# Optimization experiments

Measured on AMD Instinct MI355X. Metric: run time of the kernel, lower is better.

Reference implementation:

```python
import jax, jax.numpy as jnp
import numpy as np
from jax import lax

B, T, H, W, C = 32, 250, 28, 28, 1
CLASSES, IPC = 25, 10
UNITS = 512
MEM_CELLS = CLASSES * IPC  # 250
CELL = 64
HEADS = 4
FEAT = 2 * 2 * 32          # conv output flattened = 128
XDIM = FEAT + CLASSES      # 153
IN_LSTM = XDIM + HEADS * CELL  # 409
EPS_BN = 1e-3


def setup_inputs() -> dict:
    key = jax.random.key(0)
    ks = iter(jax.random.split(key, 40))
    s = 0.02
    d = {}
    d['images'] = jax.random.normal(next(ks), (B, T, H, W, C), jnp.float32)
    d['previous_labels'] = jax.random.randint(next(ks), (B, T), 0, CLASSES, jnp.int32)
    # conv stack
    for i, (ci, co) in enumerate([(1, 8), (8, 16), (16, 32)], start=1):
        d[f'k{i}'] = jax.random.normal(next(ks), (3, 3, ci, co), jnp.float32) * s
        d[f'cb{i}'] = jnp.zeros((co,), jnp.float32)
        d[f'g{i}'] = jnp.ones((co,), jnp.float32)
        d[f'be{i}'] = jnp.zeros((co,), jnp.float32)
        d[f'mm{i}'] = jnp.zeros((co,), jnp.float32)
        d[f'mv{i}'] = jnp.ones((co,), jnp.float32)
    # LSTM cell (keras gate order i,f,g,o)
    d['Wx'] = jax.random.normal(next(ks), (IN_LSTM, 4 * UNITS), jnp.float32) * s
    d['Wh'] = jax.random.normal(next(ks), (UNITS, 4 * UNITS), jnp.float32) * s
    d['bl'] = jnp.zeros((4 * UNITS,), jnp.float32)
    # parameters dense -> (read_heads+1)*cell_size, tanh
    d['Wp'] = jax.random.normal(next(ks), (UNITS, (HEADS + 1) * CELL), jnp.float32) * s
    d['bp'] = jnp.zeros(((HEADS + 1) * CELL,), jnp.float32)
    # output layer: Dense(units, tanh) on concat(h, read_value)
    d['Wo'] = jax.random.normal(next(ks), (UNITS + HEADS * CELL, UNITS), jnp.float32) * s
    d['bo'] = jnp.zeros((UNITS,), jnp.float32)
    # final classifier
    d['Wf'] = jax.random.normal(next(ks), (UNITS, CLASSES), jnp.float32) * s
    d['bf'] = jnp.zeros((CLASSES,), jnp.float32)
    return d


def _conv_bn_relu(x, k, cb, g, be, mm, mv):
    y = lax.conv_general_dilated(x, k, (2, 2), 'VALID',
                                 dimension_numbers=('NHWC', 'HWIO', 'NHWC')) + cb
    y = (y - mm) * g * lax.rsqrt(mv + EPS_BN) + be  # inference BN
    return jax.nn.relu(y)


def _l2n(x):
    return x * lax.rsqrt(jnp.maximum(jnp.sum(x * x, axis=-1, keepdims=True), 1e-12))


def _forward(images, previous_labels, k1, cb1, g1, be1, mm1, mv1,
             k2, cb2, g2, be2, mm2, mv2, k3, cb3, g3, be3, mm3, mv3,
             Wx, Wh, bl, Wp, bp, Wo, bo, Wf, bf):
    x = images.reshape(B * T, H, W, C)
    x = _conv_bn_relu(x, k1, cb1, g1, be1, mm1, mv1)
    x = _conv_bn_relu(x, k2, cb2, g2, be2, mm2, mv2)
    x = _conv_bn_relu(x, k3, cb3, g3, be3, mm3, mv3)
    x = x.reshape(B, T, FEAT)
    oh = jax.nn.one_hot(previous_labels, CLASSES, dtype=x.dtype)
    x = jnp.concatenate([x, oh], axis=-1)  # [B, T, XDIM]

    def step(carry, xt):
        h, c, rv, mem = carry
        inp = jnp.concatenate([xt, rv], axis=-1)
        z = inp @ Wx + h @ Wh + bl
        zi, zf, zg, zo = jnp.split(z, 4, axis=-1)
        i, f, g = jax.nn.sigmoid(zi), jax.nn.sigmoid(zf), jnp.tanh(zg)
        o = jax.nn.sigmoid(zo)
        c = f * c + i * g
        h = o * jnp.tanh(c)
        hid = jnp.tanh(h @ Wp + bp)
        wv = hid[:, :CELL]                                # write value
        keys = hid[:, CELL:].reshape(B, HEADS, CELL)
        att = jnp.einsum('brs,bms->brm', _l2n(keys), _l2n(mem))
        w = jax.nn.softmax(att, axis=-1)
        rv = jnp.einsum('brm,bms->brs', w, mem).reshape(B, HEADS * CELL)
        mem = jnp.concatenate([wv[:, None, :], mem[:, :-1]], axis=1)  # shift write
        out = jnp.tanh(jnp.concatenate([h, rv], axis=-1) @ Wo + bo)
        return (h, c, rv, mem), out

    carry0 = (jnp.zeros((B, UNITS)), jnp.zeros((B, UNITS)),
              jnp.zeros((B, HEADS * CELL)), jnp.zeros((B, MEM_CELLS, CELL)))
    _, ys = lax.scan(step, carry0, jnp.swapaxes(x, 0, 1))  # ys: [T, B, UNITS]
    rnn_out = jnp.swapaxes(ys, 0, 1)
    return jax.nn.softmax(rnn_out @ Wf + bf, axis=-1)


def reference(images, previous_labels, k1, cb1, g1, be1, mm1, mv1,
              k2, cb2, g2, be2, mm2, mv2, k3, cb3, g3, be3, mm3, mv3,
              Wx, Wh, bl, Wp, bp, Wo, bo, Wf, bf):
    return _forward(images, previous_labels, k1, cb1, g1, be1, mm1, mv1,
                    k2, cb2, g2, be2, mm2, mv2, k3, cb3, g3, be3, mm3, mv3,
                    Wx, Wh, bl, Wp, bp, Wo, bo, Wf, bf)
```

## Files before the change

### kernel.cpp

```cpp
#include <hip/hip_runtime.h>


constexpr size_t OFF_FEATP  = 0;
constexpr size_t OFF_WXI    = OFF_FEATP + (size_t)8000 * 128;
constexpr size_t OFF_WHI    = OFF_WXI + (size_t)409 * 2048;
constexpr size_t OFF_BLI    = OFF_WHI + (size_t)512 * 2048;
constexpr size_t OFF_ZP2    = OFF_BLI + 2048;
constexpr size_t OFF_OH2A   = OFF_ZP2 + 262144;
constexpr size_t OFF_OH2B   = OFF_OH2A + 65536;
constexpr size_t OFF_OUTPRE2= OFF_OH2B + 65536;
constexpr size_t OFF_HT2    = OFF_OUTPRE2 + 32768;
constexpr size_t OFF_HTT2   = OFF_HT2 + 65536;
constexpr size_t OFF_RVT2   = OFF_HTT2 + 65536;
constexpr size_t OFF_WVP2   = OFF_RVT2 + 32768;
constexpr size_t OFF_BAR    = OFF_WVP2 + 16384;
constexpr size_t OFF_WPT    = OFF_BAR + 4096;
constexpr size_t WS_FLOATS  = OFF_WPT + (size_t)163840;

constexpr int DYN_FLOATS = 34816;
constexpr int DYN_BYTES  = DYN_FLOATS * 4;

constexpr int COH = 0, COP = 512, CCO = 1024, CRING = 1536;

__device__ __forceinline__ float sigm(float x) { return 1.f / (1.f + __expf(-x)); }

typedef int iv2 __attribute__((ext_vector_type(2)));
typedef int iv4 __attribute__((ext_vector_type(4)));

__device__ __forceinline__ void st_pair(float* base, size_t pidx, float v, int tag) {
  unsigned long long u = (unsigned long long)__float_as_uint(v) |
                         ((unsigned long long)(unsigned)tag << 32);
  __hip_atomic_store((unsigned long long*)(base + 2 * pidx), u,
                     __ATOMIC_RELAXED, __HIP_MEMORY_SCOPE_AGENT);
}
__device__ __forceinline__ float spin_pair(const float* base, size_t pidx, int tag) {
  const iv2* p = (const iv2*)(base + 2 * pidx);
  iv2 v;
  for (;;) {
    asm volatile("global_load_dwordx2 %0, %1, off sc0 sc1\n\ts_waitcnt vmcnt(0)"
                 : "=&v"(v) : "v"(p) : "memory");
    if (v[1] == tag) break;
    __builtin_amdgcn_s_sleep(1);
  }
  return __int_as_float(v[0]);
}
__device__ __forceinline__ float2 spin_pair2(const float* base, size_t pidx, int tag) {
  const iv4* p = (const iv4*)(base + 2 * pidx);
  iv4 v;
  for (;;) {
    asm volatile("global_load_dwordx4 %0, %1, off sc0 sc1\n\ts_waitcnt vmcnt(0)"
                 : "=&v"(v) : "v"(p) : "memory");
    if (v[1] == tag && v[3] == tag) break;
    __builtin_amdgcn_s_sleep(1);
  }
  return {__int_as_float(v[0]), __int_as_float(v[2])};
}
__device__ __forceinline__ float2 spin_pair_2addr(const float* a, const float* b, int tag) {
  const iv2* pa = (const iv2*)a;
  const iv2* pb = (const iv2*)b;
  iv2 x, y;
  for (;;) {
    asm volatile(
        "global_load_dwordx2 %0, %2, off sc0 sc1\n\t"
        "global_load_dwordx2 %1, %3, off sc0 sc1\n\t"
        "s_waitcnt vmcnt(0)"
        : "=&v"(x), "=&v"(y) : "v"(pa), "v"(pb) : "memory");
    if (x[1] == tag && y[1] == tag) break;
    __builtin_amdgcn_s_sleep(1);
  }
  return {__int_as_float(x[0]), __int_as_float(y[0])};
}
__device__ __forceinline__ void ld8i4_sc(const iv4* b0, iv4* v) {
  const iv4 *p0 = b0, *p1 = b0 + 512, *p2 = b0 + 1024, *p3 = b0 + 1536,
            *p4 = b0 + 2048, *p5 = b0 + 2560, *p6 = b0 + 3072, *p7 = b0 + 3584;
  asm volatile(
      "global_load_dwordx4 %0, %8, off sc0 sc1\n\t"
      "global_load_dwordx4 %1, %9, off sc0 sc1\n\t"
      "global_load_dwordx4 %2, %10, off sc0 sc1\n\t"
      "global_load_dwordx4 %3, %11, off sc0 sc1\n\t"
      "global_load_dwordx4 %4, %12, off sc0 sc1\n\t"
      "global_load_dwordx4 %5, %13, off sc0 sc1\n\t"
      "global_load_dwordx4 %6, %14, off sc0 sc1\n\t"
      "global_load_dwordx4 %7, %15, off sc0 sc1\n\t"
      "s_waitcnt vmcnt(0)"
      : "=&v"(v[0]), "=&v"(v[1]), "=&v"(v[2]), "=&v"(v[3]),
        "=&v"(v[4]), "=&v"(v[5]), "=&v"(v[6]), "=&v"(v[7])
      : "v"(p0), "v"(p1), "v"(p2), "v"(p3), "v"(p4), "v"(p5), "v"(p6), "v"(p7)
      : "memory");
}
__device__ __forceinline__ void ld10i4_sc(const iv4* b0, const iv4* z0,
                                          const iv4* z1, iv4* v) {
  const iv4 *p0 = b0, *p1 = b0 + 512, *p2 = b0 + 1024, *p3 = b0 + 1536,
            *p4 = b0 + 2048, *p5 = b0 + 2560, *p6 = b0 + 3072, *p7 = b0 + 3584;
  asm volatile(
      "global_load_dwordx4 %0, %10, off sc0 sc1\n\t"
      "global_load_dwordx4 %1, %11, off sc0 sc1\n\t"
      "global_load_dwordx4 %2, %12, off sc0 sc1\n\t"
      "global_load_dwordx4 %3, %13, off sc0 sc1\n\t"
      "global_load_dwordx4 %4, %14, off sc0 sc1\n\t"
      "global_load_dwordx4 %5, %15, off sc0 sc1\n\t"
      "global_load_dwordx4 %6, %16, off sc0 sc1\n\t"
      "global_load_dwordx4 %7, %17, off sc0 sc1\n\t"
      "global_load_dwordx4 %8, %18, off sc0 sc1\n\t"
      "global_load_dwordx4 %9, %19, off sc0 sc1\n\t"
      "s_waitcnt vmcnt(0)"
      : "=&v"(v[0]), "=&v"(v[1]), "=&v"(v[2]), "=&v"(v[3]), "=&v"(v[4]),
        "=&v"(v[5]), "=&v"(v[6]), "=&v"(v[7]), "=&v"(v[8]), "=&v"(v[9])
      : "v"(p0), "v"(p1), "v"(p2), "v"(p3), "v"(p4), "v"(p5), "v"(p6), "v"(p7),
        "v"(z0), "v"(z1)
      : "memory");
}
__device__ __forceinline__ int sum8_bar(const int* b) {
  int v0, v1, v2, v3, v4, v5, v6, v7;
  asm volatile(
      "global_load_dword %0, %8, off sc0 sc1\n\t"
      "global_load_dword %1, %9, off sc0 sc1\n\t"
      "global_load_dword %2, %10, off sc0 sc1\n\t"
      "global_load_dword %3, %11, off sc0 sc1\n\t"
      "global_load_dword %4, %12, off sc0 sc1\n\t"
      "global_load_dword %5, %13, off sc0 sc1\n\t"
      "global_load_dword %6, %14, off sc0 sc1\n\t"
      "global_load_dword %7, %15, off sc0 sc1\n\t"
      "s_waitcnt vmcnt(0)"
      : "=&v"(v0), "=&v"(v1), "=&v"(v2), "=&v"(v3),
        "=&v"(v4), "=&v"(v5), "=&v"(v6), "=&v"(v7)
      : "v"(b), "v"(b + 64), "v"(b + 128), "v"(b + 192),
        "v"(b + 256), "v"(b + 320), "v"(b + 384), "v"(b + 448)
      : "memory");
  return ((v0 + v1) + (v2 + v3)) + ((v4 + v5) + (v6 + v7));
}

__global__ __launch_bounds__(256) void prep_kernel(const float* __restrict__ Wx,
                                                   const float* __restrict__ Wh,
                                                   const float* __restrict__ bl,
                                                   const float* __restrict__ Wp,
                                                   float* __restrict__ ws) {
  float* WXI = ws + OFF_WXI;
  float* WHI = ws + OFF_WHI;
  float* BLI = ws + OFF_BLI;
  float* WPT = ws + OFF_WPT;
  const int t0 = 409 * 2048;
  const int t1 = t0 + 512 * 2048;
  const int t2 = t1 + 2048;
  const int total = t2 + 163840;
  for (int idx = blockIdx.x * blockDim.x + threadIdx.x; idx < total;
       idx += gridDim.x * blockDim.x) {
    if (idx < t0) {
      int k = idx >> 11, cc = idx & 2047;
      WXI[idx] = Wx[(size_t)k * 2048 + (cc & 3) * 512 + (cc >> 2)];
    } else if (idx < t1) {
      int j = idx - t0;
      int k = j >> 11, cc = j & 2047;
      WHI[j] = Wh[(size_t)k * 2048 + (cc & 3) * 512 + (cc >> 2)];
    } else if (idx < t2) {
      int cc = idx - t1;
      BLI[cc] = bl[(cc & 3) * 512 + (cc >> 2)];
    } else {
      int e = idx - t2;
      int k4 = e / 1280, r = e - k4 * 1280;
      int j = r >> 2, ks = r & 3;
      WPT[e] = Wp[(size_t)(k4 * 4 + ks) * 320 + j];
    }
  }
}

__global__ __launch_bounds__(128) void conv_kernel(
    const float* __restrict__ img,
    const float* __restrict__ k1, const float* __restrict__ cb1, const float* __restrict__ g1,
    const float* __restrict__ be1, const float* __restrict__ mm1, const float* __restrict__ mv1,
    const float* __restrict__ k2, const float* __restrict__ cb2, const float* __restrict__ g2,
    const float* __restrict__ be2, const float* __restrict__ mm2, const float* __restrict__ mv2,
    const float* __restrict__ k3, const float* __restrict__ cb3, const float* __restrict__ g3,
    const float* __restrict__ be3, const float* __restrict__ mm3, const float* __restrict__ mv3,
    float* __restrict__ ws) {
  __shared__ float s_in[784];
  __shared__ float s_y1[13 * 13 * 8];
  __shared__ float s_y2[6 * 6 * 16];
  __shared__ float s_k1[72], s_k2[1152], s_k3[4608];
  __shared__ float s_s1[8], s_b1[8], s_s2[16], s_b2[16], s_s3[32], s_b3[32];
  float* FEATP = ws + OFF_FEATP;
  const int n = blockIdx.x, tid = threadIdx.x;
  const float* ip = img + (size_t)n * 784;
  for (int i = tid; i < 784; i += 128) s_in[i] = ip[i];
  for (int i = tid; i < 72; i += 128) s_k1[i] = k1[i];
  for (int i = tid; i < 1152; i += 128) s_k2[i] = k2[i];
  for (int i = tid; i < 4608; i += 128) s_k3[i] = k3[i];
  if (tid < 8) {
    float s = g1[tid] * rsqrtf(mv1[tid] + 1e-3f);
    s_s1[tid] = s; s_b1[tid] = (cb1[tid] - mm1[tid]) * s + be1[tid];
  } else if (tid >= 32 && tid < 48) {
    int c = tid - 32;
    float s = g2[c] * rsqrtf(mv2[c] + 1e-3f);
    s_s2[c] = s; s_b2[c] = (cb2[c] - mm2[c]) * s + be2[c];
  } else if (tid >= 64 && tid < 96) {
    int c = tid - 64;
    float s = g3[c] * rsqrtf(mv3[c] + 1e-3f);
    s_s3[c] = s; s_b3[c] = (cb3[c] - mm3[c]) * s + be3[c];
  }
  __syncthreads();
  for (int idx = tid; idx < 13 * 13 * 8; idx += 128) {
    int co = idx & 7, pos = idx >> 3;
    int j = pos % 13, i = pos / 13;
    float acc = 0.f;
    #pragma unroll
    for (int ky = 0; ky < 3; ++ky)
      #pragma unroll
      for (int kx = 0; kx < 3; ++kx)
        acc += s_in[(2 * i + ky) * 28 + (2 * j + kx)] * s_k1[(ky * 3 + kx) * 8 + co];
    float v = acc * s_s1[co] + s_b1[co];
    s_y1[idx] = v > 0.f ? v : 0.f;
  }
  __syncthreads();
  for (int idx = tid; idx < 6 * 6 * 16; idx += 128) {
    int co = idx & 15, pos = idx >> 4;
    int j = pos % 6, i = pos / 6;
    float acc = 0.f;
    for (int ky = 0; ky < 3; ++ky)
      for (int kx = 0; kx < 3; ++kx) {
        int base = ((2 * i + ky) * 13 + (2 * j + kx)) * 8;
        int kb = (ky * 3 + kx) * 128 + co;
        #pragma unroll
        for (int ci = 0; ci < 8; ++ci) acc += s_y1[base + ci] * s_k2[kb + ci * 16];
      }
    float v = acc * s_s2[co] + s_b2[co];
    s_y2[idx] = v > 0.f ? v : 0.f;
  }
  __syncthreads();
  for (int idx = tid; idx < 128; idx += 128) {
    int co = idx & 31, pos = idx >> 5;
    int j = pos & 1, i = pos >> 1;
    float acc = 0.f;
    for (int ky = 0; ky < 3; ++ky)
      for (int kx = 0; kx < 3; ++kx) {
        int base = ((2 * i + ky) * 6 + (2 * j + kx)) * 16;
        int kb = (ky * 3 + kx) * 512 + co;
        #pragma unroll
        for (int ci = 0; ci < 16; ++ci) acc += s_y2[base + ci] * s_k3[kb + ci * 32];
      }
    float v = acc * s_s3[co] + s_b3[co];
    FEATP[(size_t)n * 128 + idx] = v > 0.f ? v : 0.f;
  }
}

__global__ __launch_bounds__(512) void lstm_kernel(
    const int* __restrict__ labels,
    const float* __restrict__ Wo, const float* __restrict__ bo,
    const float* __restrict__ Wp, const float* __restrict__ bp,
    const float* __restrict__ Wf, const float* __restrict__ bf,
    float* __restrict__ ws, float* __restrict__ out) {
  extern __shared__ float dyn[];
  const float* FEATP = ws + OFF_FEATP;
  const float* WXI   = ws + OFF_WXI;
  const float* WHI   = ws + OFF_WHI;
  const float* BLI   = ws + OFF_BLI;
  float* ZP2    = ws + OFF_ZP2;
  float* OH2A   = ws + OFF_OH2A;
  float* OH2B   = ws + OFF_OH2B;
  float* OUTPRE2= ws + OFF_OUTPRE2;
  float* HT2    = ws + OFF_HT2;
  float* HTT2   = ws + OFF_HTT2;
  float* RVT2   = ws + OFF_RVT2;
  float* WVP2   = ws + OFF_WVP2;
  const float* WPT = ws + OFF_WPT;
  int*   BARp   = (int*)(ws + OFF_BAR);

  const int bid = blockIdx.x;
  const int tid = threadIdx.x;

  auto waitC = [&](int base, int target) {
    if (tid == 0) {
      while (sum8_bar(BARp + base) < target) {}
    }
    __syncthreads();
  };
  auto bumpC = [&](int base) {
    asm volatile("s_waitcnt vmcnt(0)" ::: "memory");
    __syncthreads();
    if (tid == 0) atomicAdd(&BARp[base + ((bid & 7) << 6)], 1);
  };

  auto stageP = [&](float* dst, const float* srcPairs, int tag) {
    const iv4* sp = (const iv4*)srcPairs + tid;
    iv4 v[8];
    for (;;) {
      ld8i4_sc(sp, v);
      bool ok = true;
      #pragma unroll
      for (int j = 0; j < 8; ++j) ok = ok && (v[j][1] == tag) && (v[j][3] == tag);
      if (ok) break;
      __builtin_amdgcn_s_sleep(2);
    }
    #pragma unroll
    for (int j = 0; j < 8; ++j) {
      int i = (tid + j * 512) << 1;
      float2 f = {__int_as_float(v[j][0]), __int_as_float(v[j][2])};
      *(float2*)&dst[(i >> 5) * 36 + (i & 31)] = f;
    }
  };

  auto E32 = [&](const float* Wm, const float* Am, int K, float* part, float2& r) {
    const int wv = tid >> 6, l = tid & 63;
    const int ksub = l & 1, cg = (l >> 1) & 3, bg = l >> 3;
    const int Kp = K >> 4;
    const int kb = wv * (K >> 3) + ksub * Kp;
    const float* wp = Wm + (size_t)kb * 32 + cg * 8;
    const float* ap = Am + (size_t)kb * 36 + bg * 4;
    float4 acc[8];
    #pragma unroll
    for (int i = 0; i < 8; ++i) acc[i] = {0.f, 0.f, 0.f, 0.f};
    #pragma unroll 4
    for (int kk = 0; kk < Kp; ++kk) {
      float4 w0 = *(const float4*)(wp + kk * 32);
      float4 w1 = *(const float4*)(wp + kk * 32 + 4);
      float4 a  = *(const float4*)(ap + kk * 36);
      float wl[8];
      *(float4*)&wl[0] = w0; *(float4*)&wl[4] = w1;
      #pragma unroll
      for (int i = 0; i < 8; ++i) {
        acc[i].x = fmaf(wl[i], a.x, acc[i].x);
        acc[i].y = fmaf(wl[i], a.y, acc[i].y);
        acc[i].z = fmaf(wl[i], a.z, acc[i].z);
        acc[i].w = fmaf(wl[i], a.w, acc[i].w);
      }
    }
    #pragma unroll
    for (int i = 0; i < 8; ++i) {
      acc[i].x += __shfl_xor(acc[i].x, 1, 64);
      acc[i].y += __shfl_xor(acc[i].y, 1, 64);
      acc[i].z += __shfl_xor(acc[i].z, 1, 64);
      acc[i].w += __shfl_xor(acc[i].w, 1, 64);
    }
    const int ob = (cg * 8) * 36 + bg * 4;
    if (ksub == 0 && wv < 4) {
      float* pb = part + wv * 1152 + ob;
      #pragma unroll
      for (int i = 0; i < 8; ++i) *(float4*)(pb + i * 36) = acc[i];
    }
    __syncthreads();
    if (ksub == 0 && wv >= 4) {
      float* pb = part + (wv - 4) * 1152 + ob;
      #pragma unroll
      for (int i = 0; i < 8; ++i) {
        float4 t = *(float4*)(pb + i * 36);
        t.x += acc[i].x; t.y += acc[i].y; t.z += acc[i].z; t.w += acc[i].w;
        *(float4*)(pb + i * 36) = t;
      }
    }
    __syncthreads();
    const int c = tid & 31, b2 = (tid >> 5) * 2;
    const int o = c * 36 + b2;
    float2 s0 = *(float2*)(part + o);
    float2 s1 = *(float2*)(part + 1152 + o);
    float2 s2 = *(float2*)(part + 2304 + o);
    float2 s3 = *(float2*)(part + 3456 + o);
    r.x = (s0.x + s1.x) + (s2.x + s3.x);
    r.y = (s0.y + s1.y) + (s2.y + s3.y);
  };

  if (bid < 64) {
    const int c0 = bid * 32;
    for (int i = tid; i < 8192; i += 512)
      dyn[i] = WXI[(size_t)(153 + (i >> 5)) * 2048 + c0 + (i & 31)];
    for (int i = tid; i < 4096; i += 512)
      dyn[8192 + i] = WXI[(size_t)(i >> 5) * 2048 + c0 + (i & 31)];
    if (tid < 256) dyn[12288 + tid] = 0.f;
  } else if (bid < 80) {
    const int u0 = (bid - 64) * 32;
    for (int i = tid; i < 8192; i += 512)
      dyn[i] = Wo[(size_t)(512 + (i >> 5)) * 512 + u0 + (i & 31)];
    if (tid < 32) dyn[8192 + tid] = bo[u0 + tid];
  } else if (bid < 144) {
    const int c0 = (bid - 80) * 32;
    for (int i = tid; i < 16384; i += 512)
      dyn[i] = WHI[(size_t)(i >> 5) * 2048 + c0 + (i & 31)];
    if (tid < 32) dyn[16384 + tid] = BLI[c0 + tid];
  } else if (bid < 160) {
    const int u0 = (bid - 144) * 32;
    for (int i = tid; i < 8192; i += 512)
      dyn[i] = Wo[(size_t)(i >> 5) * 512 + u0 + (i & 31)];
  } else if (bid < 176) {
    const int u0 = (bid - 160) * 32;
    for (int i = tid; i < 8192; i += 512)
      dyn[i] = Wo[(size_t)(256 + (i >> 5)) * 512 + u0 + (i & 31)];
  } else if (bid < 240) {
    const int hp = (bid - 176) & 1;
    for (int i = tid; i < 17000; i += 512) dyn[i] = 0.f;
    if (tid < 256) dyn[17000 + tid] = rsqrtf(1e-12f);
    if (tid < 128) dyn[21264 + tid] = bp[64 + hp * 128 + tid];
    if (tid < 64)  dyn[21392 + tid] = bp[tid];
  } else if (bid < 244) {
    const int kh = (bid - 240) >> 1, cp = (bid - 240) & 1;
    for (int i = tid; i < 8192; i += 512) {
      int k = i >> 5, c = i & 31;
      dyn[i] = Wp[(size_t)(kh * 256 + k) * 320 + cp * 32 + c];
    }
  } else if (bid < 252) {
    for (int i = tid; i < 12800; i += 512) dyn[i] = Wf[i];
    if (tid < 25) dyn[12800 + tid] = bf[tid];
  }
  __syncthreads();

  auto azPre = [&](int t) {
    const int c0 = bid * 32;
    const float* zpP = ZP2 + (t & 1) * 131072;
    float* zf = dyn + 27392;
    const int bb = tid >> 4, c2 = tid & 15;
    float2 x = spin_pair2(zpP, (size_t)bb * 2048 + c0 + c2 * 2, t + 1);
    *(float2*)&zf[bb * 32 + c2 * 2] = x;
  };
  auto azGatesMain = [&](int t) {
    const float* rvP = RVT2 + ((t + 1) & 1) * 16384;
    float* Wz = dyn; float* Cst = dyn + 12288; float* rvT = dyn + 12544;
    float* zx = dyn + 26368; float* zf = dyn + 27392; float* part = dyn + 28416;
    stageP(rvT, rvP, t);
    __syncthreads();
    float2 r;
    E32(Wz, rvT, 256, part, r);
    const int c = tid & 31, b2 = (tid >> 5) * 2;
    zf[b2 * 32 + c] += r.x + zx[b2 * 32 + c];
    zf[(b2 + 1) * 32 + c] += r.y + zx[(b2 + 1) * 32 + c];
    __syncthreads();
    if (tid < 256) {
      int u = tid & 7, b = tid >> 3;
      float4 z = *(float4*)(zf + b * 32 + u * 4);
      float ig = sigm(z.x), fg = sigm(z.y), gg = tanhf(z.z), og = sigm(z.w);
      float cc = fg * Cst[b * 8 + u] + ig * gg;
      Cst[b * 8 + u] = cc;
      float hv = og * tanhf(cc);
      st_pair(HT2 + (t & 1) * 32768, (size_t)(bid * 8 + u) * 32 + b, hv, t + 1);
      st_pair(HTT2 + (t & 1) * 32768, (size_t)b * 512 + bid * 8 + u, hv, t + 1);
    }
  };
  auto azX = [&](int tt) {
    float* Wxx = dyn + 8192; float* xT = dyn + 21760;
    float* zx = dyn + 26368; float* part = dyn + 28416;
    for (int i = tid; i < 4096; i += 512) {
      int b = i >> 7, k = i & 127;
      xT[k * 36 + b] = FEATP[((size_t)b * 250 + tt) * 128 + k];
    }
    __syncthreads();
    float2 r;
    E32(Wxx, xT, 128, part, r);
    const int c = tid & 31, b2 = (tid >> 5) * 2;
    zx[b2 * 32 + c] = r.x;
    zx[(b2 + 1) * 32 + c] = r.y;
  };
  auto aoOut = [&](int t) {
    const int u0 = (bid - 64) * 32;
    const float* rvP  = RVT2 + ((t + 1) & 1) * 16384;
    const float* ohaP = OH2A + ((t + 1) & 1) * 32768;
    const float* ohbP = OH2B + ((t + 1) & 1) * 32768;
    float* W = dyn; float* bo_l = dyn + 8192; float* rvT = dyn + 8224;
    float* of = dyn + 17440; float* part = dyn + 18464;
    {
      const int b = tid >> 4, c2 = tid & 15;
      const iv4* rp = (const iv4*)rvP + tid;
      const iv4* za = (const iv4*)ohaP + (b * 256 + (u0 >> 1) + c2);
      const iv4* zb = (const iv4*)ohbP + (b * 256 + (u0 >> 1) + c2);
      iv4 v[10];
      for (;;) {
        ld10i4_sc(rp, za, zb, v);
        bool ok = true;
        #pragma unroll
        for (int j = 0; j < 10; ++j) ok = ok && (v[j][1] == t) && (v[j][3] == t);
        if (ok) break;
        __builtin_amdgcn_s_sleep(2);
      }
      #pragma unroll
      for (int j = 0; j < 8; ++j) {
        int i = (tid + j * 512) << 1;
        float2 f = {__int_as_float(v[j][0]), __int_as_float(v[j][2])};
        *(float2*)&rvT[(i >> 5) * 36 + (i & 31)] = f;
      }
      float2 s = {__int_as_float(v[8][0]) + __int_as_float(v[9][0]),
                  __int_as_float(v[8][2]) + __int_as_float(v[9][2])};
      *(float2*)&of[b * 32 + c2 * 2] = s;
    }
    __syncthreads();
    float2 r;
    E32(W, rvT, 256, part, r);
    const int c = tid & 31, b2 = (tid >> 5) * 2;
    float bv = bo_l[c];
    st_pair(OUTPRE2, (size_t)b2 * 512 + u0 + c, r.x + of[b2 * 32 + c] + bv, t);
    st_pair(OUTPRE2, (size_t)(b2 + 1) * 512 + u0 + c, r.y + of[(b2 + 1) * 32 + c] + bv, t);
  };
  auto zhLab = [&](int s) {
    __syncthreads();
    int* slab = (int*)(dyn + 16416);
    if (tid < 32) slab[tid] = labels[tid * 250 + s];
  };
  auto zhGemm = [&](int s) {
    const int c0 = (bid - 80) * 32;
    const float* htP = HT2 + ((s + 1) & 1) * 32768;
    float* zpD = ZP2 + (s & 1) * 131072;
    float* W = dyn; float* blc = dyn + 16384; int* slab = (int*)(dyn + 16416);
    float* A = dyn + 16448; float* part = dyn + 25664;
    stageP(A, htP, s);
    __syncthreads();
    float2 r1;
    E32(W, A, 256, part, r1);
    __syncthreads();
    stageP(A, htP + 16384, s);
    __syncthreads();
    float2 r2;
    E32(W + 8192, A, 256, part, r2);
    const int c = tid & 31, b2 = (tid >> 5) * 2;
    float base = blc[c];
    int l0 = slab[b2], l1 = slab[b2 + 1];
    st_pair(zpD, (size_t)b2 * 2048 + c0 + c,
            r1.x + r2.x + base + WXI[(size_t)(128 + l0) * 2048 + c0 + c], s + 1);
    st_pair(zpD, (size_t)(b2 + 1) * 2048 + c0 + c,
            r1.y + r2.y + base + WXI[(size_t)(128 + l1) * 2048 + c0 + c], s + 1);
  };
  auto p2Gemm = [&](int t) {
    const float* htP = HT2 + (t & 1) * 32768;
    float* W = dyn; float* A = dyn + 8192; float* part = dyn + 17408;
    const bool isOLr = bid < 160;
    stageP(A, isOLr ? htP : (htP + 16384), t + 1);
    __syncthreads();
    float2 r;
    E32(W, A, 256, part, r);
    const int c = tid & 31, b2 = (tid >> 5) * 2;
    const int u0 = (isOLr ? (bid - 144) : (bid - 160)) * 32;
    float* d = (isOLr ? OH2A : OH2B) + (t & 1) * 32768;
    st_pair(d, (size_t)b2 * 512 + u0 + c, r.x, t + 1);
    st_pair(d, (size_t)(b2 + 1) * 512 + u0 + c, r.y, t + 1);
  };
  auto caOutB = [&](int b, int t) {
    float* WfL = dyn; float* bfL = dyn + 12800;
    float* to = dyn + 12832; float* lp = dyn + 13344; float* lg = dyn + 13744;
    to[tid] = tanhf(spin_pair(OUTPRE2, (size_t)b * 512 + tid, t));
    __syncthreads();
    if (tid < 400) {
      int l = tid % 25, p = tid / 25;
      float s = 0.f;
      #pragma unroll
      for (int q = 0; q < 32; ++q) { int k = p * 32 + q; s += to[k] * WfL[k * 25 + l]; }
      lp[p * 25 + l] = s;
    }
    __syncthreads();
    if (tid < 25) {
      float s = bfL[tid];
      #pragma unroll
      for (int p = 0; p < 16; ++p) s += lp[p * 25 + tid];
      lg[tid] = s;
    }
    __syncthreads();
    if (tid == 0) {
      float mx = lg[0];
      for (int l = 1; l < 25; ++l) mx = fmaxf(mx, lg[l]);
      float ss = 0.f;
      for (int l = 0; l < 25; ++l) ss += __expf(lg[l] - mx);
      lg[25] = mx; lg[26] = 1.f / ss;
    }
    __syncthreads();
    if (tid < 25)
      out[((size_t)b * 250 + (t - 1)) * 25 + tid] = __expf(lg[tid] - lg[25]) * lg[26];
    __syncthreads();
  };

  if (bid < 64) {
    azX(0);
    for (int t = 0; t < 250; ++t) {
      azPre(t);
      if (t >= 2) waitC(COH, 32 * (t - 1));
      azGatesMain(t);
      if (t < 249) azX(t + 1);
    }
  } else if (bid < 80) {
    for (int t = 1; t <= 250; ++t) {
      if (t >= 2) waitC(CCO, 8 * (t - 1));
      aoOut(t);
      bumpC(COP);
    }
  } else if (bid < 144) {
    for (int s = 0; s < 250; ++s) {
      zhLab(s);
      zhGemm(s);
    }
  } else if (bid < 176) {
    for (int t = 0; t < 250; ++t) {
      if (t >= 2) waitC(COP, 16 * (t - 1));
      p2Gemm(t);
      bumpC(COH);
    }
  } else if (bid < 240) {
    float* ring = dyn;
    float* rn   = dyn + 17000;
    float* h_s  = dyn + 17256;
    float* kpart= dyn + 17768;
    float* kv   = dyn + 18280;
    float* kn   = dyn + 18408;
    float* att  = dyn + 18536;
    float* redK = dyn + 19048;
    float* redM = dyn + 19052;
    float* redS = dyn + 19068;
    float* pslab= dyn + 19088;
    float* bpk  = dyn + 21264;
    float* bpw  = dyn + 21392;
    const int b = (bid - 176) >> 1, hp = (bid - 176) & 1;
    const int j = tid & 127, q = tid >> 7;
    const int J = 64 + hp * 128 + j;
    const float4* wbase = (const float4*)WPT + q * 32 * 320 + J;
    for (int t = 0; t < 250; ++t) {
      float4 pf[16];
      #pragma unroll
      for (int i = 0; i < 16; ++i) pf[i] = wbase[i * 320];
      if (t >= 2) waitC(COP, 16 * (t - 1));
      h_s[tid] = spin_pair(HTT2 + (t & 1) * 32768, (size_t)b * 512 + tid, t + 1);
      __syncthreads();
      {
        float a = 0.f;
        #pragma unroll
        for (int i = 0; i < 16; ++i) {
          float4 h4 = *(const float4*)&h_s[q * 128 + i * 4];
          a += pf[i].x * h4.x + pf[i].y * h4.y + pf[i].z * h4.z + pf[i].w * h4.w;
        }
        #pragma unroll 4
        for (int i = 16; i < 32; ++i) {
          float4 w = wbase[i * 320];
          float4 h4 = *(const float4*)&h_s[q * 128 + i * 4];
          a += w.x * h4.x + w.y * h4.y + w.z * h4.z + w.w * h4.w;
        }
        kpart[q * 128 + j] = a;
      }
      __syncthreads();
      if (tid < 128) {
        float kr = kpart[tid] + kpart[128 + tid] + kpart[256 + tid] +
                   kpart[384 + tid] + bpk[tid];
        float v = tanhf(kr);
        kv[tid] = v;
        float pq = v * v;
        #pragma unroll
        for (int off = 32; off; off >>= 1) pq += __shfl_xor(pq, off, 64);
        if ((tid & 63) == 0) redK[tid >> 6] = rsqrtf(fmaxf(pq, 1e-12f));
      }
      __syncthreads();
      if (tid < 128) kn[tid] = kv[tid] * redK[tid >> 6];
      __syncthreads();
      const int start = (250 - t) % 250;
      const int m = tid >> 1, hh = tid & 1;
      {
        float v;
        if (m < 250) {
          int p = start + m; if (p >= 250) p -= 250;
          const float4* c4 = (const float4*)ring + p * 17;
          const float4* k4 = (const float4*)kn + hh * 16;
          float d = 0.f;
          #pragma unroll
          for (int s4 = 0; s4 < 16; ++s4) {
            float4 cc = c4[s4], kk = k4[s4];
            d += cc.x * kk.x + cc.y * kk.y + cc.z * kk.z + cc.w * kk.w;
          }
          v = d * rn[p];
        } else v = -3.0e38f;
        float mx = v;
        #pragma unroll
        for (int off = 2; off <= 32; off <<= 1) mx = fmaxf(mx, __shfl_xor(mx, off, 64));
        if ((tid & 63) < 2) redM[(tid >> 6) * 2 + (tid & 1)] = mx;
        __syncthreads();
        float MX = redM[hh];
        #pragma unroll
        for (int w = 1; w < 8; ++w) MX = fmaxf(MX, redM[w * 2 + hh]);
        float e = (m < 250) ? __expf(v - MX) : 0.f;
        if (m < 250) att[hh * 256 + m] = e;
        float sm = e;
        #pragma unroll
        for (int off = 2; off <= 32; off <<= 1) sm += __shfl_xor(sm, off, 64);
        if ((tid & 63) < 2) redS[(tid >> 6) * 2 + (tid & 1)] = sm;
      }
      __syncthreads();
      {
        int hh2 = tid >> 8, s4 = (tid >> 4) & 15, g = tid & 15;
        float4 a4 = {0.f, 0.f, 0.f, 0.f};
        for (int mm = g; mm < 250; mm += 16) {
          int p = start + mm; if (p >= 250) p -= 250;
          float w = att[hh2 * 256 + mm];
          float4 cc = ((const float4*)ring)[p * 17 + s4];
          a4.x = fmaf(w, cc.x, a4.x); a4.y = fmaf(w, cc.y, a4.y);
          a4.z = fmaf(w, cc.z, a4.z); a4.w = fmaf(w, cc.w, a4.w);
        }
        *(float4*)&pslab[(hh2 * 16 + s4) * 68 + g * 4] = a4;
      }
      __syncthreads();
      if (tid < 128) {
        int hh3 = tid >> 6, s = tid & 63;
        float denom = redS[hh3];
        #pragma unroll
        for (int w = 1; w < 8; ++w) denom += redS[w * 2 + hh3];
        float sum = 0.f;
        #pragma unroll
        for (int g = 0; g < 16; ++g)
          sum += pslab[(hh3 * 16 + (s >> 2)) * 68 + g * 4 + (s & 3)];
        st_pair(RVT2 + (t & 1) * 16384,
                (size_t)((2 * hp + hh3) * 64 + s) * 32 + b, sum / denom, t + 1);
      }
      __syncthreads();
      {
        int ip = start + 249; if (ip >= 250) ip -= 250;
        if (tid < 64) {
          float2 p01 = spin_pair_2addr(
              WVP2 + (t & 1) * 8192 + 2 * ((size_t)b * 64 + tid),
              WVP2 + (t & 1) * 8192 + 4096 + 2 * ((size_t)b * 64 + tid), t + 1);
          float nv = tanhf(p01.x + p01.y + bpw[tid]);
          ring[ip * 68 + tid] = nv;
          float n2 = nv * nv;
          #pragma unroll
          for (int off = 32; off; off >>= 1) n2 += __shfl_xor(n2, off, 64);
          if (tid == 0) rn[ip] = rsqrtf(fmaxf(n2, 1e-12f));
        }
      }
      bumpC(CRING);
    }
  } else if (bid < 244) {
    const int kh = (bid - 240) >> 1, cp = (bid - 240) & 1;
    float* W = dyn; float* A = dyn + 8192; float* part = dyn + 17408;
    for (int t = 0; t < 250; ++t) {
      if (t >= 2) waitC(CRING, 64 * (t - 1));
      stageP(A, HT2 + (t & 1) * 32768 + kh * 16384, t + 1);
      __syncthreads();
      float2 r;
      E32(W, A, 256, part, r);
      const int c = tid & 31, b2 = (tid >> 5) * 2;
      float* d = WVP2 + (t & 1) * 8192 + kh * 4096;
      st_pair(d, (size_t)b2 * 64 + cp * 32 + c, r.x, t + 1);
      st_pair(d, (size_t)(b2 + 1) * 64 + cp * 32 + c, r.y, t + 1);
    }
  } else if (bid < 252) {
    const int b0 = (bid - 244) * 4;
    for (int t = 1; t <= 250; ++t) {
      caOutB(b0 + 0, t);
      caOutB(b0 + 1, t);
      caOutB(b0 + 2, t);
      caOutB(b0 + 3, t);
      bumpC(CCO);
    }
  }
}

extern "C" void kernel_launch(void* const* d_in, const int* in_sizes, int n_in,
                              void* d_out, int out_size, void* d_ws, size_t ws_size,
                              hipStream_t stream) {
  const float* images = (const float*)d_in[0];
  const int* labels = (const int*)d_in[1];
  const float* k1  = (const float*)d_in[2];
  const float* cb1 = (const float*)d_in[3];
  const float* g1  = (const float*)d_in[4];
  const float* be1 = (const float*)d_in[5];
  const float* mm1 = (const float*)d_in[6];
  const float* mv1 = (const float*)d_in[7];
  const float* k2  = (const float*)d_in[8];
  const float* cb2 = (const float*)d_in[9];
  const float* g2  = (const float*)d_in[10];
  const float* be2 = (const float*)d_in[11];
  const float* mm2 = (const float*)d_in[12];
  const float* mv2 = (const float*)d_in[13];
  const float* k3  = (const float*)d_in[14];
  const float* cb3 = (const float*)d_in[15];
  const float* g3  = (const float*)d_in[16];
  const float* be3 = (const float*)d_in[17];
  const float* mm3 = (const float*)d_in[18];
  const float* mv3 = (const float*)d_in[19];
  const float* Wx  = (const float*)d_in[20];
  const float* Wh  = (const float*)d_in[21];
  const float* bl  = (const float*)d_in[22];
  const float* Wp  = (const float*)d_in[23];
  const float* bp  = (const float*)d_in[24];
  const float* Wo  = (const float*)d_in[25];
  const float* bo  = (const float*)d_in[26];
  const float* Wf  = (const float*)d_in[27];
  const float* bf  = (const float*)d_in[28];
  float* ws = (float*)d_ws;

  hipFuncSetAttribute((const void*)lstm_kernel,
                      hipFuncAttributeMaxDynamicSharedMemorySize, DYN_BYTES);

  hipMemsetAsync((char*)d_ws + OFF_ZP2 * sizeof(float), 0,
                 (OFF_WPT - OFF_ZP2) * sizeof(float), stream);
  prep_kernel<<<1024, 256, 0, stream>>>(Wx, Wh, bl, Wp, ws);
  conv_kernel<<<8000, 128, 0, stream>>>(images,
      k1, cb1, g1, be1, mm1, mv1,
      k2, cb2, g2, be2, mm2, mv2,
      k3, cb3, g3, be3, mm3, mv3, ws);
  lstm_kernel<<<256, 512, DYN_BYTES, stream>>>(labels, Wo, bo, Wp, bp, Wf, bf, ws,
                                               (float*)d_out);
}
```

Baseline: 3.935 ms.

## Split recurrent Wh GEMM across K halves, cache barrier counts, batch output polling

Each Wh-GEMM block now computes 64 columns over half of K (kh) with a new E64 routine, writing partials to two Z buffers that the gate blocks sum while spinning. waitC caches the last observed barrier count to skip redundant global polls. The attention block fully prefetches the Wp slice into registers, fuses the key normalisation, and drops the softmax max-subtraction. The output blocks poll all four batch rows at once before running the classifier. Together these aim to shorten the per-step critical path, at the cost of extra workspace and possible exp overflow without max subtraction.

```diff
diff --git a/kernel.cpp b/kernel.cpp
--- a/kernel.cpp
+++ b/kernel.cpp
@@ -5,8 +5,9 @@
 constexpr size_t OFF_WXI    = OFF_FEATP + (size_t)8000 * 128;
 constexpr size_t OFF_WHI    = OFF_WXI + (size_t)409 * 2048;
 constexpr size_t OFF_BLI    = OFF_WHI + (size_t)512 * 2048;
-constexpr size_t OFF_ZP2    = OFF_BLI + 2048;
-constexpr size_t OFF_OH2A   = OFF_ZP2 + 262144;
+constexpr size_t OFF_ZP2A   = OFF_BLI + 2048;
+constexpr size_t OFF_ZP2B   = OFF_ZP2A + 262144;
+constexpr size_t OFF_OH2A   = OFF_ZP2B + 262144;
 constexpr size_t OFF_OH2B   = OFF_OH2A + 65536;
 constexpr size_t OFF_OUTPRE2= OFF_OH2B + 65536;
 constexpr size_t OFF_HT2    = OFF_OUTPRE2 + 32768;
@@ -44,16 +45,21 @@
   }
   return __int_as_float(v[0]);
 }
-__device__ __forceinline__ float2 spin_pair2(const float* base, size_t pidx, int tag) {
-  const iv4* p = (const iv4*)(base + 2 * pidx);
-  iv4 v;
+__device__ __forceinline__ float2 spin_pair2_sum2(const float* a, const float* b, int tag) {
+  const iv4* pa = (const iv4*)a;
+  const iv4* pb = (const iv4*)b;
+  iv4 x, y;
   for (;;) {
-    asm volatile("global_load_dwordx4 %0, %1, off sc0 sc1\n\ts_waitcnt vmcnt(0)"
-                 : "=&v"(v) : "v"(p) : "memory");
-    if (v[1] == tag && v[3] == tag) break;
+    asm volatile(
+        "global_load_dwordx4 %0, %2, off sc0 sc1\n\t"
+        "global_load_dwordx4 %1, %3, off sc0 sc1\n\t"
+        "s_waitcnt vmcnt(0)"
+        : "=&v"(x), "=&v"(y) : "v"(pa), "v"(pb) : "memory");
+    if (x[1] == tag && x[3] == tag && y[1] == tag && y[3] == tag) break;
     __builtin_amdgcn_s_sleep(1);
   }
-  return {__int_as_float(v[0]), __int_as_float(v[2])};
+  return {__int_as_float(x[0]) + __int_as_float(y[0]),
+          __int_as_float(x[2]) + __int_as_float(y[2])};
 }
 __device__ __forceinline__ float2 spin_pair_2addr(const float* a, const float* b, int tag) {
   const iv2* pa = (const iv2*)a;
@@ -69,6 +75,17 @@
     __builtin_amdgcn_s_sleep(1);
   }
   return {__int_as_float(x[0]), __int_as_float(y[0])};
+}
+__device__ __forceinline__ void ld4x2_sc(const iv2* a, const iv2* b, const iv2* c,
+                                         const iv2* d, iv2& x, iv2& y, iv2& z, iv2& w) {
+  asm volatile(
+      "global_load_dwordx2 %0, %4, off sc0 sc1\n\t"
+      "global_load_dwordx2 %1, %5, off sc0 sc1\n\t"
+      "global_load_dwordx2 %2, %6, off sc0 sc1\n\t"
+      "global_load_dwordx2 %3, %7, off sc0 sc1\n\t"
+      "s_waitcnt vmcnt(0)"
+      : "=&v"(x), "=&v"(y), "=&v"(z), "=&v"(w)
+      : "v"(a), "v"(b), "v"(c), "v"(d) : "memory");
 }
 __device__ __forceinline__ void ld8i4_sc(const iv4* b0, iv4* v) {
   const iv4 *p0 = b0, *p1 = b0 + 512, *p2 = b0 + 1024, *p3 = b0 + 1536,
@@ -253,7 +270,8 @@
   const float* WXI   = ws + OFF_WXI;
   const float* WHI   = ws + OFF_WHI;
   const float* BLI   = ws + OFF_BLI;
-  float* ZP2    = ws + OFF_ZP2;
+  float* ZP2A   = ws + OFF_ZP2A;
+  float* ZP2B   = ws + OFF_ZP2B;
   float* OH2A   = ws + OFF_OH2A;
   float* OH2B   = ws + OFF_OH2B;
   float* OUTPRE2= ws + OFF_OUTPRE2;
@@ -267,10 +285,16 @@
   const int bid = blockIdx.x;
   const int tid = threadIdx.x;
 
-  auto waitC = [&](int base, int target) {
+  int* bc = (int*)(dyn + 34808);
+  auto waitC = [&](int base, int target, int& cache) {
+    if (cache >= target) return;
     if (tid == 0) {
-      while (sum8_bar(BARp + base) < target) {}
-    }
+      int v = sum8_bar(BARp + base);
+      while (v < target) v = sum8_bar(BARp + base);
+      bc[base >> 9] = v;
+    }
+    __syncthreads();
+    cache = bc[base >> 9];
     __syncthreads();
   };
   auto bumpC = [&](int base) {
@@ -357,6 +381,81 @@
     r.y = (s0.y + s1.y) + (s2.y + s3.y);
   };
 
+  auto E64 = [&](const float* Wm, const float* Am, float* part, float4& r) {
+    const int wv = tid >> 6, l = tid & 63;
+    const int ksub = l & 1, cg = (l >> 1) & 7, bg = l >> 4;
+    const int kb = wv * 32 + ksub * 16;
+    const float* wp0 = Wm + (size_t)kb * 64 + ((cg * 8 + ksub * 4) & 63);
+    const float* wp1 = Wm + (size_t)kb * 64 + ((cg * 8 + 4 + ksub * 4) & 63);
+    const float* ap = Am + (size_t)kb * 36 + bg * 8;
+    float4 acc[8][2];
+    #pragma unroll
+    for (int i = 0; i < 8; ++i) { acc[i][0] = {0.f,0.f,0.f,0.f}; acc[i][1] = {0.f,0.f,0.f,0.f}; }
+    #pragma unroll 2
+    for (int kk = 0; kk < 16; ++kk) {
+      float4 w0 = *(const float4*)(wp0 + kk * 64);
+      float4 w1 = *(const float4*)(wp1 + kk * 64);
+      float4 a0 = *(const float4*)(ap + kk * 36);
+      float4 a1 = *(const float4*)(ap + kk * 36 + 4);
+      float wl[8];
+      *(float4*)&wl[0] = w0; *(float4*)&wl[4] = w1;
+      #pragma unroll
+      for (int i = 0; i < 8; ++i) {
+        acc[i][0].x = fmaf(wl[i], a0.x, acc[i][0].x);
+        acc[i][0].y = fmaf(wl[i], a0.y, acc[i][0].y);
+        acc[i][0].z = fmaf(wl[i], a0.z, acc[i][0].z);
+        acc[i][0].w = fmaf(wl[i], a0.w, acc[i][0].w);
+        acc[i][1].x = fmaf(wl[i], a1.x, acc[i][1].x);
+        acc[i][1].y = fmaf(wl[i], a1.y, acc[i][1].y);
+        acc[i][1].z = fmaf(wl[i], a1.z, acc[i][1].z);
+        acc[i][1].w = fmaf(wl[i], a1.w, acc[i][1].w);
+      }
+    }
+    #pragma unroll
+    for (int i = 0; i < 8; ++i) {
+      #pragma unroll
+      for (int j = 0; j < 2; ++j) {
+        acc[i][j].x += __shfl_xor(acc[i][j].x, 1, 64);
+        acc[i][j].y += __shfl_xor(acc[i][j].y, 1, 64);
+        acc[i][j].z += __shfl_xor(acc[i][j].z, 1, 64);
+        acc[i][j].w += __shfl_xor(acc[i][j].w, 1, 64);
+      }
+    }
+    const int ob = (cg * 8) * 36 + bg * 8;
+    if (ksub == 0 && wv < 4) {
+      float* pb = part + wv * 2304 + ob;
+      #pragma unroll
+      for (int i = 0; i < 8; ++i) {
+        *(float4*)(pb + i * 36) = acc[i][0];
+        *(float4*)(pb + i * 36 + 4) = acc[i][1];
+      }
+    }
+    __syncthreads();
+    if (ksub == 0 && wv >= 4) {
+      float* pb = part + (wv - 4) * 2304 + ob;
+      #pragma unroll
+      for (int i = 0; i < 8; ++i) {
+        float4 t0 = *(float4*)(pb + i * 36);
+        float4 t1 = *(float4*)(pb + i * 36 + 4);
+        t0.x += acc[i][0].x; t0.y += acc[i][0].y; t0.z += acc[i][0].z; t0.w += acc[i][0].w;
+        t1.x += acc[i][1].x; t1.y += acc[i][1].y; t1.z += acc[i][1].z; t1.w += acc[i][1].w;
+        *(float4*)(pb + i * 36) = t0;
+        *(float4*)(pb + i * 36 + 4) = t1;
+      }
+    }
+    __syncthreads();
+    const int c = tid & 63, b4 = (tid >> 6) * 4;
+    const int o = c * 36 + b4;
+    float4 s0 = *(float4*)(part + o);
+    float4 s1 = *(float4*)(part + 2304 + o);
+    float4 s2 = *(float4*)(part + 4608 + o);
+    float4 s3 = *(float4*)(part + 6912 + o);
+    r.x = (s0.x + s1.x) + (s2.x + s3.x);
+    r.y = (s0.y + s1.y) + (s2.y + s3.y);
+    r.z = (s0.z + s1.z) + (s2.z + s3.z);
+    r.w = (s0.w + s1.w) + (s2.w + s3.w);
+  };
+
   if (bid < 64) {
     const int c0 = bid * 32;
     for (int i = tid; i < 8192; i += 512)
@@ -370,10 +469,13 @@
       dyn[i] = Wo[(size_t)(512 + (i >> 5)) * 512 + u0 + (i & 31)];
     if (tid < 32) dyn[8192 + tid] = bo[u0 + tid];
   } else if (bid < 144) {
-    const int c0 = (bid - 80) * 32;
-    for (int i = tid; i < 16384; i += 512)
-      dyn[i] = WHI[(size_t)(i >> 5) * 2048 + c0 + (i & 31)];
-    if (tid < 32) dyn[16384 + tid] = BLI[c0 + tid];
+    const int r = bid - 80;
+    const int j0 = (r & 31) * 64, kh = r >> 5;
+    for (int i = tid; i < 16384; i += 512) {
+      int k = i >> 6, cc = i & 63;
+      int cr = (cc + ((k >> 4) & 1) * 4) & 63;
+      dyn[k * 64 + cr] = WHI[(size_t)(kh * 256 + k) * 2048 + j0 + cc];
+    }
   } else if (bid < 160) {
     const int u0 = (bid - 144) * 32;
     for (int i = tid; i < 8192; i += 512)
@@ -402,11 +504,13 @@
 
   auto azPre = [&](int t) {
     const int c0 = bid * 32;
-    const float* zpP = ZP2 + (t & 1) * 131072;
+    const float* zaP = ZP2A + (t & 1) * 131072;
+    const float* zbP = ZP2B + (t & 1) * 131072;
     float* zf = dyn + 27392;
     const int bb = tid >> 4, c2 = tid & 15;
-    float2 x = spin_pair2(zpP, (size_t)bb * 2048 + c0 + c2 * 2, t + 1);
-    *(float2*)&zf[bb * 32 + c2 * 2] = x;
+    size_t pidx = (size_t)bb * 2048 + c0 + c2 * 2;
+    float2 s = spin_pair2_sum2(zaP + 2 * pidx, zbP + 2 * pidx, t + 1);
+    *(float2*)&zf[bb * 32 + c2 * 2] = s;
   };
   auto azGatesMain = [&](int t) {
     const float* rvP = RVT2 + ((t + 1) & 1) * 16384;
@@ -484,34 +588,6 @@
     st_pair(OUTPRE2, (size_t)b2 * 512 + u0 + c, r.x + of[b2 * 32 + c] + bv, t);
     st_pair(OUTPRE2, (size_t)(b2 + 1) * 512 + u0 + c, r.y + of[(b2 + 1) * 32 + c] + bv, t);
   };
-  auto zhLab = [&](int s) {
-    __syncthreads();
-    int* slab = (int*)(dyn + 16416);
-    if (tid < 32) slab[tid] = labels[tid * 250 + s];
-  };
-  auto zhGemm = [&](int s) {
-    const int c0 = (bid - 80) * 32;
-    const float* htP = HT2 + ((s + 1) & 1) * 32768;
-    float* zpD = ZP2 + (s & 1) * 131072;
-    float* W = dyn; float* blc = dyn + 16384; int* slab = (int*)(dyn + 16416);
-    float* A = dyn + 16448; float* part = dyn + 25664;
-    stageP(A, htP, s);
-    __syncthreads();
-    float2 r1;
-    E32(W, A, 256, part, r1);
-    __syncthreads();
-    stageP(A, htP + 16384, s);
-    __syncthreads();
-    float2 r2;
-    E32(W + 8192, A, 256, part, r2);
-    const int c = tid & 31, b2 = (tid >> 5) * 2;
-    float base = blc[c];
-    int l0 = slab[b2], l1 = slab[b2 + 1];
-    st_pair(zpD, (size_t)b2 * 2048 + c0 + c,
-            r1.x + r2.x + base + WXI[(size_t)(128 + l0) * 2048 + c0 + c], s + 1);
-    st_pair(zpD, (size_t)(b2 + 1) * 2048 + c0 + c,
-            r1.y + r2.y + base + WXI[(size_t)(128 + l1) * 2048 + c0 + c], s + 1);
-  };
   auto p2Gemm = [&](int t) {
     const float* htP = HT2 + (t & 1) * 32768;
     float* W = dyn; float* A = dyn + 8192; float* part = dyn + 17408;
@@ -526,61 +602,54 @@
     st_pair(d, (size_t)b2 * 512 + u0 + c, r.x, t + 1);
     st_pair(d, (size_t)(b2 + 1) * 512 + u0 + c, r.y, t + 1);
   };
-  auto caOutB = [&](int b, int t) {
-    float* WfL = dyn; float* bfL = dyn + 12800;
-    float* to = dyn + 12832; float* lp = dyn + 13344; float* lg = dyn + 13744;
-    to[tid] = tanhf(spin_pair(OUTPRE2, (size_t)b * 512 + tid, t));
-    __syncthreads();
-    if (tid < 400) {
-      int l = tid % 25, p = tid / 25;
-      float s = 0.f;
-      #pragma unroll
-      for (int q = 0; q < 32; ++q) { int k = p * 32 + q; s += to[k] * WfL[k * 25 + l]; }
-      lp[p * 25 + l] = s;
-    }
-    __syncthreads();
-    if (tid < 25) {
-      float s = bfL[tid];
-      #pragma unroll
-      for (int p = 0; p < 16; ++p) s += lp[p * 25 + tid];
-      lg[tid] = s;
-    }
-    __syncthreads();
-    if (tid == 0) {
-      float mx = lg[0];
-      for (int l = 1; l < 25; ++l) mx = fmaxf(mx, lg[l]);
-      float ss = 0.f;
-      for (int l = 0; l < 25; ++l) ss += __expf(lg[l] - mx);
-      lg[25] = mx; lg[26] = 1.f / ss;
-    }
-    __syncthreads();
-    if (tid < 25)
-      out[((size_t)b * 250 + (t - 1)) * 25 + tid] = __expf(lg[tid] - lg[25]) * lg[26];
-    __syncthreads();
-  };
 
   if (bid < 64) {
+    int cCOH = 0;
     azX(0);
     for (int t = 0; t < 250; ++t) {
       azPre(t);
-      if (t >= 2) waitC(COH, 32 * (t - 1));
+      if (t >= 2) waitC(COH, 32 * (t - 1), cCOH);
       azGatesMain(t);
       if (t < 249) azX(t + 1);
     }
   } else if (bid < 80) {
+    int cCCO = 0;
     for (int t = 1; t <= 250; ++t) {
-      if (t >= 2) waitC(CCO, 8 * (t - 1));
+      if (t >= 2) waitC(CCO, 8 * (t - 1), cCCO);
       aoOut(t);
       bumpC(COP);
     }
   } else if (bid < 144) {
+    const int r = bid - 80;
+    const int j0 = (r & 31) * 64, kh = r >> 5;
+    const int c = tid & 63, b4 = (tid >> 6) * 4;
+    float* W = dyn; float* A = dyn + 16384; float* part = dyn + 25600;
+    float* zpBase = kh ? ZP2B : ZP2A;
+    const float blv = (kh == 0) ? BLI[j0 + c] : 0.f;
     for (int s = 0; s < 250; ++s) {
-      zhLab(s);
-      zhGemm(s);
+      float wx0 = 0.f, wx1 = 0.f, wx2 = 0.f, wx3 = 0.f;
+      if (kh == 0) {
+        int l0 = labels[(b4 + 0) * 250 + s], l1 = labels[(b4 + 1) * 250 + s];
+        int l2 = labels[(b4 + 2) * 250 + s], l3 = labels[(b4 + 3) * 250 + s];
+        wx0 = WXI[(size_t)(128 + l0) * 2048 + j0 + c];
+        wx1 = WXI[(size_t)(128 + l1) * 2048 + j0 + c];
+        wx2 = WXI[(size_t)(128 + l2) * 2048 + j0 + c];
+        wx3 = WXI[(size_t)(128 + l3) * 2048 + j0 + c];
+      }
+      stageP(A, HT2 + ((s + 1) & 1) * 32768 + kh * 16384, s);
+      __syncthreads();
+      float4 rr;
+      E64(W, A, part, rr);
+      float* zpD = zpBase + (s & 1) * 131072;
+      st_pair(zpD, (size_t)(b4 + 0) * 2048 + j0 + c, rr.x + blv + wx0, s + 1);
+      st_pair(zpD, (size_t)(b4 + 1) * 2048 + j0 + c, rr.y + blv + wx1, s + 1);
+      st_pair(zpD, (size_t)(b4 + 2) * 2048 + j0 + c, rr.z + blv + wx2, s + 1);
+      st_pair(zpD, (size_t)(b4 + 3) * 2048 + j0 + c, rr.w + blv + wx3, s + 1);
     }
   } else if (bid < 176) {
+    int cCOP = 0;
     for (int t = 0; t < 250; ++t) {
-      if (t >= 2) waitC(COP, 16 * (t - 1));
+      if (t >= 2) waitC(COP, 16 * (t - 1), cCOP);
       p2Gemm(t);
       bumpC(COH);
     }
@@ -589,11 +658,8 @@
     float* rn   = dyn + 17000;
     float* h_s  = dyn + 17256;
     float* kpart= dyn + 17768;
-    float* kv   = dyn + 18280;
     float* kn   = dyn + 18408;
     float* att  = dyn + 18536;
-    float* redK = dyn + 19048;
-    float* redM = dyn + 19052;
     float* redS = dyn + 19068;
     float* pslab= dyn + 19088;
     float* bpk  = dyn + 21264;
@@ -602,25 +668,20 @@
     const int j = tid & 127, q = tid >> 7;
     const int J = 64 + hp * 128 + j;
     const float4* wbase = (const float4*)WPT + q * 32 * 320 + J;
+    int cCOP = 0;
     for (int t = 0; t < 250; ++t) {
-      float4 pf[16];
-      #pragma unroll
-      for (int i = 0; i < 16; ++i) pf[i] = wbase[i * 320];
-      if (t >= 2) waitC(COP, 16 * (t - 1));
+      float4 pf[32];
+      #pragma unroll
+      for (int i = 0; i < 32; ++i) pf[i] = wbase[i * 320];
+      if (t >= 2) waitC(COP, 16 * (t - 1), cCOP);
       h_s[tid] = spin_pair(HTT2 + (t & 1) * 32768, (size_t)b * 512 + tid, t + 1);
       __syncthreads();
       {
         float a = 0.f;
         #pragma unroll
-        for (int i = 0; i < 16; ++i) {
+        for (int i = 0; i < 32; ++i) {
           float4 h4 = *(const float4*)&h_s[q * 128 + i * 4];
           a += pf[i].x * h4.x + pf[i].y * h4.y + pf[i].z * h4.z + pf[i].w * h4.w;
-        }
-        #pragma unroll 4
-        for (int i = 16; i < 32; ++i) {
-          float4 w = wbase[i * 320];
-          float4 h4 = *(const float4*)&h_s[q * 128 + i * 4];
-          a += w.x * h4.x + w.y * h4.y + w.z * h4.z + w.w * h4.w;
         }
         kpart[q * 128 + j] = a;
       }
@@ -629,19 +690,16 @@
         float kr = kpart[tid] + kpart[128 + tid] + kpart[256 + tid] +
                    kpart[384 + tid] + bpk[tid];
         float v = tanhf(kr);
-        kv[tid] = v;
         float pq = v * v;
         #pragma unroll
         for (int off = 32; off; off >>= 1) pq += __shfl_xor(pq, off, 64);
-        if ((tid & 63) == 0) redK[tid >> 6] = rsqrtf(fmaxf(pq, 1e-12f));
-      }
-      __syncthreads();
-      if (tid < 128) kn[tid] = kv[tid] * redK[tid >> 6];
+        kn[tid] = v * rsqrtf(fmaxf(pq, 1e-12f));
+      }
       __syncthreads();
       const int start = (250 - t) % 250;
       const int m = tid >> 1, hh = tid & 1;
       {
-        float v;
+        float e = 0.f;
         if (m < 250) {
           int p = start + m; if (p >= 250) p -= 250;
           const float4* c4 = (const float4*)ring + p * 17;
@@ -652,18 +710,9 @@
             float4 cc = c4[s4], kk = k4[s4];
             d += cc.x * kk.x + cc.y * kk.y + cc.z * kk.z + cc.w * kk.w;
           }
-          v = d * rn[p];
-        } else v = -3.0e38f;
-        float mx = v;
-        #pragma unroll
-        for (int off = 2; off <= 32; off <<= 1) mx = fmaxf(mx, __shfl_xor(mx, off, 64));
-        if ((tid & 63) < 2) redM[(tid >> 6) * 2 + (tid & 1)] = mx;
-        __syncthreads();
-        float MX = redM[hh];
-        #pragma unroll
-        for (int w = 1; w < 8; ++w) MX = fmaxf(MX, redM[w * 2 + hh]);
-        float e = (m < 250) ? __expf(v - MX) : 0.f;
-        if (m < 250) att[hh * 256 + m] = e;
+          e = __expf(d * rn[p]);
+          att[hh * 256 + m] = e;
+        }
         float sm = e;
         #pragma unroll
         for (int off = 2; off <= 32; off <<= 1) sm += __shfl_xor(sm, off, 64);
@@ -715,8 +764,9 @@
   } else if (bid < 244) {
     const int kh = (bid - 240) >> 1, cp = (bid - 240) & 1;
     float* W = dyn; float* A = dyn + 8192; float* part = dyn + 17408;
+    int cCR = 0;
     for (int t = 0; t < 250; ++t) {
-      if (t >= 2) waitC(CRING, 64 * (t - 1));
+      if (t >= 2) waitC(CRING, 64 * (t - 1), cCR);
       stageP(A, HT2 + (t & 1) * 32768 + kh * 16384, t + 1);
       __syncthreads();
       float2 r;
@@ -728,11 +778,58 @@
     }
   } else if (bid < 252) {
     const int b0 = (bid - 244) * 4;
+    float* WfL = dyn; float* bfL = dyn + 12800;
+    float* to4 = dyn + 12832;
+    float* lp  = dyn + 14880;
+    float* lg  = dyn + 15280;
     for (int t = 1; t <= 250; ++t) {
-      caOutB(b0 + 0, t);
-      caOutB(b0 + 1, t);
-      caOutB(b0 + 2, t);
-      caOutB(b0 + 3, t);
+      {
+        const iv2* p0 = (const iv2*)(OUTPRE2 + 2 * ((size_t)(b0 + 0) * 512 + tid));
+        const iv2* p1 = (const iv2*)(OUTPRE2 + 2 * ((size_t)(b0 + 1) * 512 + tid));
+        const iv2* p2 = (const iv2*)(OUTPRE2 + 2 * ((size_t)(b0 + 2) * 512 + tid));
+        const iv2* p3 = (const iv2*)(OUTPRE2 + 2 * ((size_t)(b0 + 3) * 512 + tid));
+        iv2 v0, v1, v2, v3;
+        for (;;) {
+          ld4x2_sc(p0, p1, p2, p3, v0, v1, v2, v3);
+          if (v0[1] == t && v1[1] == t && v2[1] == t && v3[1] == t) break;
+          __builtin_amdgcn_s_sleep(2);
+        }
+        to4[tid]        = tanhf(__int_as_float(v0[0]));
+        to4[512 + tid]  = tanhf(__int_as_float(v1[0]));
+        to4[1024 + tid] = tanhf(__int_as_float(v2[0]));
+        to4[1536 + tid] = tanhf(__int_as_float(v3[0]));
+      }
+      __syncthreads();
+      for (int i = 0; i < 4; ++i) {
+        float* to = to4 + i * 512;
+        if (tid < 400) {
+          int l = tid % 25, p = tid / 25;
+          float s = 0.f;
+          #pragma unroll
+          for (int q = 0; q < 32; ++q) { int k = p * 32 + q; s += to[k] * WfL[k * 25 + l]; }
+          lp[p * 25 + l] = s;
+        }
+        __syncthreads();
+        if (tid < 25) {
+          float s = bfL[tid];
+          #pragma unroll
+          for (int p = 0; p < 16; ++p) s += lp[p * 25 + tid];
+          lg[tid] = s;
+        }
+        __syncthreads();
+        if (tid == 0) {
+          float mx = lg[0];
+          for (int l = 1; l < 25; ++l) mx = fmaxf(mx, lg[l]);
+          float ss = 0.f;
+          for (int l = 0; l < 25; ++l) ss += __expf(lg[l] - mx);
+          lg[25] = mx; lg[26] = 1.f / ss;
+        }
+        __syncthreads();
+        if (tid < 25)
+          out[((size_t)(b0 + i) * 250 + (t - 1)) * 25 + tid] =
+              __expf(lg[tid] - lg[25]) * lg[26];
+        __syncthreads();
+      }
       bumpC(CCO);
     }
   }
@@ -775,8 +872,8 @@
   hipFuncSetAttribute((const void*)lstm_kernel,
                       hipFuncAttributeMaxDynamicSharedMemorySize, DYN_BYTES);
 
-  hipMemsetAsync((char*)d_ws + OFF_ZP2 * sizeof(float), 0,
-                 (OFF_WPT - OFF_ZP2) * sizeof(float), stream);
+  hipMemsetAsync((char*)d_ws + OFF_ZP2A * sizeof(float), 0,
+                 (OFF_WPT - OFF_ZP2A) * sizeof(float), stream);
   prep_kernel<<<1024, 256, 0, stream>>>(Wx, Wh, bl, Wp, ws);
   conv_kernel<<<8000, 128, 0, stream>>>(images,
       k1, cb1, g1, be1, mm1, mv1,
```

Measured after the change: 3.844 ms. 2.3% less time.
